# Kernel optimization log

Hardware: AMD Instinct MI355X
Metric: run time of the kernel (lower is better)

Reference implementation:

```python
import jax, jax.numpy as jnp
from jax import lax
import numpy as np

K = 9  # 3x3 kernel taps


def _mdconv(x, w, off_w, off_b):
    # Modulated deformable conv v2, kernel 3x3, stride 1, pad 1, no bias.
    N, C, H, W = x.shape
    # offset/mask predictor: plain 3x3 conv -> 27 channels (18 offsets + 9 mask)
    off = lax.conv_general_dilated(x, off_w, (1, 1), ((1, 1), (1, 1))) + off_b[None, :, None, None]
    o = off[:, :2 * K].reshape(N, K, 2, H, W)  # channel 2k = dy_k, 2k+1 = dx_k
    dy, dx = o[:, :, 0], o[:, :, 1]            # [N,K,H,W]
    m = jax.nn.sigmoid(off[:, 2 * K:])          # modulation mask [N,K,H,W]
    ky = jnp.arange(K) // 3 - 1                 # kernel tap row offsets
    kx = jnp.arange(K) % 3 - 1
    py = dy + ky[None, :, None, None] + jnp.arange(H)[None, None, :, None]
    px = dx + kx[None, :, None, None] + jnp.arange(W)[None, None, None, :]
    y0 = jnp.floor(py)
    x0 = jnp.floor(px)
    ly = py - y0
    lx = px - x0
    y0i = y0.astype(jnp.int32)
    x0i = x0.astype(jnp.int32)
    x_flat = x.reshape(N, C, H * W)

    def corner(yi, xi, wgt):
        valid = (yi >= 0) & (yi < H) & (xi >= 0) & (xi < W)  # zero padding outside
        idx = jnp.clip(yi, 0, H - 1) * W + jnp.clip(xi, 0, W - 1)  # [N,K,H,W]
        g = jax.vmap(lambda xf, ix: xf[:, ix.reshape(-1)])(x_flat, idx)
        g = g.reshape(N, C, K, H, W)
        return g * (wgt * valid)[:, None]

    s = (corner(y0i, x0i, (1 - ly) * (1 - lx))
         + corner(y0i, x0i + 1, (1 - ly) * lx)
         + corner(y0i + 1, x0i, ly * (1 - lx))
         + corner(y0i + 1, x0i + 1, ly * lx))
    s = s * m[:, None]  # modulate sampled values
    return jnp.einsum('nckhw,ock->nohw', s, w.reshape(w.shape[0], C, K))


def _bn_relu(x, g, b, eps=1e-5):
    # training-mode BatchNorm2d (batch statistics over N,H,W) + ReLU
    mu = x.mean((0, 2, 3), keepdims=True)
    var = ((x - mu) ** 2).mean((0, 2, 3), keepdims=True)
    return jax.nn.relu((x - mu) * lax.rsqrt(var + eps) * g[None, :, None, None] + b[None, :, None, None])


def setup_inputs() -> dict:
    key = jax.random.key(0)
    ks = jax.random.split(key, 5)
    N, Cin, Cmid, Cout, H, W = 4, 64, 128, 128, 96, 96
    x = jax.random.normal(ks[0], (N, Cin, H, W), jnp.float32)
    w1 = jax.random.normal(ks[1], (Cmid, Cin, 3, 3), jnp.float32) * 0.06   # ~kaiming scale
    w2 = jax.random.normal(ks[2], (Cout, Cmid, 3, 3), jnp.float32) * 0.04
    off_w1 = jax.random.normal(ks[3], (27, Cin, 3, 3), jnp.float32) * 0.01  # small offsets
    off_w2 = jax.random.normal(ks[4], (27, Cmid, 3, 3), jnp.float32) * 0.01
    return {
        'x': x,
        'w1': w1, 'off_w1': off_w1, 'off_b1': jnp.zeros((27,), jnp.float32),
        'gamma1': jnp.ones((Cmid,), jnp.float32), 'beta1': jnp.zeros((Cmid,), jnp.float32),
        'w2': w2, 'off_w2': off_w2, 'off_b2': jnp.zeros((27,), jnp.float32),
        'gamma2': jnp.ones((Cout,), jnp.float32), 'beta2': jnp.zeros((Cout,), jnp.float32),
    }


def reference(x, w1, off_w1, off_b1, gamma1, beta1, w2, off_w2, off_b2, gamma2, beta2):
    h = _bn_relu(_mdconv(x, w1, off_w1, off_b1), gamma1, beta1)
    return _bn_relu(_mdconv(h, w2, off_w2, off_b2), gamma2, beta2)
```

## Files before the change

kernel.cpp:

```cpp
#include <hip/hip_runtime.h>
#include <math.h>

#define N_  4
#define H_  96
#define W_  96
#define HW  9216
#define NHW 36864
#define O_  128
#define PW  98
#define PHW 9604

typedef unsigned short ushort_t;
typedef __attribute__((ext_vector_type(8))) short bf16x8;
typedef __attribute__((ext_vector_type(4))) float f32x4;
typedef __attribute__((ext_vector_type(8))) unsigned short u16x8;

__device__ __forceinline__ float bf2f(ushort_t u) {
  return __uint_as_float(((unsigned int)u) << 16);
}
__device__ __forceinline__ ushort_t f2bf(float f) {
  unsigned int u = __float_as_uint(f);
  u += 0x7fffu + ((u >> 16) & 1u);
  return (ushort_t)(u >> 16);
}

__global__ __launch_bounds__(256) void to_nhwc_pad_kernel(const float* __restrict__ x,
                                                          ushort_t* __restrict__ xp, int C) {
  __shared__ ushort_t L[32][33];
  int ctiles = C >> 5;
  int b = blockIdx.x;
  int ct = b % ctiles;
  int hwt = (b / ctiles) % (HW / 32);
  int n = b / (ctiles * (HW / 32));
  int tx = threadIdx.x & 31, ty = threadIdx.x >> 5;
#pragma unroll
  for (int i = 0; i < 4; ++i) {
    int cl = ty + i * 8;
    L[cl][tx] = f2bf(x[((size_t)(n * C + ct * 32 + cl)) * HW + hwt * 32 + tx]);
  }
  __syncthreads();
#pragma unroll
  for (int i = 0; i < 4; ++i) {
    int hl = ty + i * 8;
    int hw = hwt * 32 + hl;
    int y = hw / W_, xx = hw % W_;
    xp[((size_t)n * PHW + (y + 1) * PW + (xx + 1)) * C + ct * 32 + tx] = L[tx][hl];
  }
}

__global__ void transpose_w_kernel(const float* __restrict__ w,
                                   ushort_t* __restrict__ wB, int C) {
  int K = C * 9;
  int i = blockIdx.x * 256 + threadIdx.x;
  if (i >= 128 * K) return;
  int o = i / K, r = i % K;
  int kk = r / C, c = r % C;
  wB[i] = f2bf(w[(o * C + c) * 9 + kk]);
}

__global__ void transpose_wo_kernel(const float* __restrict__ ow,
                                    ushort_t* __restrict__ wOB, int C) {
  int K = C * 9;
  int i = blockIdx.x * 256 + threadIdx.x;
  if (i >= 32 * K) return;
  int o = i / K, r = i % K;
  int kk = r / C, c = r % C;
  wOB[i] = (o < 27) ? f2bf(ow[(o * C + c) * 9 + kk]) : (ushort_t)0;
}

__device__ __forceinline__ void gll16(const ushort_t* g, ushort_t* l) {
  __builtin_amdgcn_global_load_lds((const __attribute__((address_space(1))) void*)g,
                                   (__attribute__((address_space(3))) void*)l, 16, 0, 0);
}
__device__ __forceinline__ int swz(int row) {
  return (row & 3) ^ ((row >> 2) & 3);
}

template <int C>
__global__ __launch_bounds__(256) void gemm_off_kernel(
    const ushort_t* __restrict__ xp, const ushort_t* __restrict__ B,
    const float* __restrict__ ob, float* __restrict__ offt, int n0) {
  constexpr int K = C * 9;
  __shared__ __align__(16) ushort_t As[64 * 32];
  __shared__ __align__(16) ushort_t Bs[32 * 32];
  int tid = threadIdx.x;
  int m0 = blockIdx.x * 64;
  int lane = tid & 63, wid = tid >> 6;
  f32x4 acc[2];
  acc[0] = (f32x4){0.f, 0.f, 0.f, 0.f};
  acc[1] = (f32x4){0.f, 0.f, 0.f, 0.f};
  int srow = tid >> 2, chl = tid & 3, q = lane >> 4;
  int mg = m0 + srow;
  int nl = mg / HW, hw = mg % HW;
  int y = hw / W_, x = hw % W_;
  const ushort_t* xn = xp + (size_t)(n0 + nl) * PHW * C;
  int pbase = ((y + 1) * PW + (x + 1)) * C;
  int chg = chl ^ swz(srow);
  for (int kt = 0; kt < K; kt += 32) {
    int kk = kt / C, c0 = kt % C;
    int shift = ((kk / 3 - 1) * PW + (kk % 3 - 1)) * C;
    gll16(xn + pbase + shift + c0 + chg * 8, As + tid * 8);
    if (tid < 128) {
      int row = tid >> 2;
      gll16(B + (size_t)row * K + kt + ((tid & 3) ^ swz(row)) * 8, Bs + tid * 8);
    }
    __syncthreads();
    int r = wid * 16 + (lane & 15);
    bf16x8 af = *reinterpret_cast<const bf16x8*>(&As[r * 32 + ((q ^ swz(r)) << 3)]);
#pragma unroll
    for (int oi = 0; oi < 2; ++oi) {
      int rb = oi * 16 + (lane & 15);
      bf16x8 bfr = *reinterpret_cast<const bf16x8*>(&Bs[rb * 32 + ((q ^ swz(rb)) << 3)]);
      acc[oi] = __builtin_amdgcn_mfma_f32_16x16x32_bf16(af, bfr, acc[oi], 0, 0, 0);
    }
    __syncthreads();
  }
#pragma unroll
  for (int oi = 0; oi < 2; ++oi) {
    int o = oi * 16 + (lane & 15);
    if (o < 27) {
      float b = ob[o];
      int mb = n0 * HW + m0 + wid * 16 + ((lane >> 4) << 2);
#pragma unroll
      for (int j = 0; j < 4; ++j)
        offt[(size_t)(mb + j) * 28 + o] = acc[oi][j] + b;
    }
  }
}

template <int C>
__global__ __launch_bounds__(256) void sample_nhwc_kernel(
    const ushort_t* __restrict__ xp, const float* __restrict__ offt,
    ushort_t* __restrict__ s, int n0) {
  constexpr int CH = C / 8;
  int g = blockIdx.x * 256 + threadIdx.x;
  int cc = g % CH;
  int t = g / CH;
  int kk = t % 9;
  int ml = t / 9;
  int nl = ml / HW, hw = ml % HW;
  int h = hw / W_, w = hw % W_;
  const float* op = offt + ((size_t)n0 * HW + ml) * 28;
  float dy = op[2 * kk];
  float dx = op[2 * kk + 1];
  float mo = op[18 + kk];
  float mm = 1.f / (1.f + __expf(-mo));
  float py = dy + (float)(kk / 3 - 1 + h);
  float px = dx + (float)(kk % 3 - 1 + w);
  float fy = floorf(py), fx = floorf(px);
  int y0 = (int)fy, x0 = (int)fx;
  float ly = py - fy, lx = px - fx;
  int y1 = y0 + 1, x1 = x0 + 1;
  bool vy0 = (y0 >= 0) & (y0 < H_), vy1 = (y1 >= 0) & (y1 < H_);
  bool vx0 = (x0 >= 0) & (x0 < W_), vx1 = (x1 >= 0) & (x1 < W_);
  int y0c = min(max(y0, 0), H_ - 1), y1c = min(max(y1, 0), H_ - 1);
  int x0c = min(max(x0, 0), W_ - 1), x1c = min(max(x1, 0), W_ - 1);
  float w00 = (vy0 & vx0) ? (1.f - ly) * (1.f - lx) * mm : 0.f;
  float w01 = (vy0 & vx1) ? (1.f - ly) * lx * mm : 0.f;
  float w10 = (vy1 & vx0) ? ly * (1.f - lx) * mm : 0.f;
  float w11 = (vy1 & vx1) ? ly * lx * mm : 0.f;
  const ushort_t* xb = xp + (size_t)(n0 + nl) * PHW * C + cc * 8;
  const ushort_t* p00 = xb + (size_t)((y0c + 1) * PW + x0c + 1) * C;
  const ushort_t* p01 = xb + (size_t)((y0c + 1) * PW + x1c + 1) * C;
  const ushort_t* p10 = xb + (size_t)((y1c + 1) * PW + x0c + 1) * C;
  const ushort_t* p11 = xb + (size_t)((y1c + 1) * PW + x1c + 1) * C;
  u16x8 a = *reinterpret_cast<const u16x8*>(p00);
  u16x8 b = *reinterpret_cast<const u16x8*>(p01);
  u16x8 c2 = *reinterpret_cast<const u16x8*>(p10);
  u16x8 d = *reinterpret_cast<const u16x8*>(p11);
  u16x8 r;
#pragma unroll
  for (int e = 0; e < 8; ++e) {
    float v = w00 * bf2f(a[e]) + w01 * bf2f(b[e])
            + w10 * bf2f(c2[e]) + w11 * bf2f(d[e]);
    r[e] = f2bf(v);
  }
  *reinterpret_cast<u16x8*>(s + ((size_t)ml * 9 + kk) * C + cc * 8) = r;
}

template <int K>
__global__ __launch_bounds__(256) void gemm_kernel(
    const ushort_t* __restrict__ A, const ushort_t* __restrict__ B,
    float* __restrict__ Y, int mbase) {
  __shared__ __align__(16) ushort_t As[64 * 32];
  __shared__ __align__(16) ushort_t Bs[128 * 32];
  int tid = threadIdx.x;
  int m0 = blockIdx.x * 64;
  int lane = tid & 63, wid = tid >> 6;
  int wr = wid >> 1, wc = wid & 1;
  f32x4 acc[2][4];
#pragma unroll
  for (int mi = 0; mi < 2; ++mi)
#pragma unroll
    for (int oi = 0; oi < 4; ++oi) acc[mi][oi] = (f32x4){0.f, 0.f, 0.f, 0.f};
  int srow = tid >> 2, chl = tid & 3, q = lane >> 4;
  for (int kt = 0; kt < K; kt += 32) {
    gll16(A + (size_t)(m0 + srow) * K + kt + (chl ^ swz(srow)) * 8, As + tid * 8);
#pragma unroll
    for (int rr = 0; rr < 2; ++rr) {
      int row = srow + 64 * rr;
      gll16(B + (size_t)row * K + kt + (chl ^ swz(row)) * 8, Bs + rr * 2048 + tid * 8);
    }
    __syncthreads();
    bf16x8 af[2], bfr[4];
#pragma unroll
    for (int mi = 0; mi < 2; ++mi) {
      int r = wr * 32 + mi * 16 + (lane & 15);
      af[mi] = *reinterpret_cast<const bf16x8*>(&As[r * 32 + ((q ^ swz(r)) << 3)]);
    }
#pragma unroll
    for (int oi = 0; oi < 4; ++oi) {
      int r = wc * 64 + oi * 16 + (lane & 15);
      bfr[oi] = *reinterpret_cast<const bf16x8*>(&Bs[r * 32 + ((q ^ swz(r)) << 3)]);
    }
#pragma unroll
    for (int mi = 0; mi < 2; ++mi)
#pragma unroll
      for (int oi = 0; oi < 4; ++oi)
        acc[mi][oi] = __builtin_amdgcn_mfma_f32_16x16x32_bf16(af[mi], bfr[oi], acc[mi][oi], 0, 0, 0);
    __syncthreads();
  }
#pragma unroll
  for (int mi = 0; mi < 2; ++mi)
#pragma unroll
    for (int oi = 0; oi < 4; ++oi) {
      int o = wc * 64 + oi * 16 + (lane & 15);
      int mb = m0 + wr * 32 + mi * 16 + ((lane >> 4) << 2);
#pragma unroll
      for (int j = 0; j < 4; ++j)
        Y[(size_t)(mbase + mb + j) * O_ + o] = acc[mi][oi][j];
    }
}

__global__ __launch_bounds__(256) void bn_stats_kernel(const float* __restrict__ Y,
                                                       float* __restrict__ stats) {
  int o = threadIdx.x & 127;
  int seg = blockIdx.x * 2 + (threadIdx.x >> 7);
  const float* p = Y + (size_t)seg * 72 * O_ + o;
  float s = 0.f, s2 = 0.f;
#pragma unroll 4
  for (int mm = 0; mm < 72; ++mm) {
    float v = p[(size_t)mm * O_];
    s += v; s2 += v * v;
  }
  atomicAdd(&stats[o], s);
  atomicAdd(&stats[128 + o], s2);
}

__global__ __launch_bounds__(256) void bn_apply_pad_kernel(
    const float* __restrict__ Y, const float* __restrict__ stats,
    const float* __restrict__ gamma, const float* __restrict__ beta,
    ushort_t* __restrict__ hp) {
  int g = blockIdx.x * 256 + threadIdx.x;
  int m = g >> 4;
  int o0 = (g & 15) * 8;
  int n = m / HW, hw = m % HW;
  int y = hw / W_, x = hw % W_;
  const float4* yp = reinterpret_cast<const float4*>(Y) + (size_t)g * 2;
  float4 a = yp[0], b = yp[1];
  float va[8] = {a.x, a.y, a.z, a.w, b.x, b.y, b.z, b.w};
  u16x8 r;
#pragma unroll
  for (int e = 0; e < 8; ++e) {
    int o = o0 + e;
    float mu = stats[o] * (1.f / (float)NHW);
    float var = stats[128 + o] * (1.f / (float)NHW) - mu * mu;
    float sc = rsqrtf(var + 1e-5f) * gamma[o];
    float sh = beta[o] - mu * sc;
    r[e] = f2bf(fmaxf(fmaf(va[e], sc, sh), 0.f));
  }
  size_t pp = ((size_t)n * PHW + (y + 1) * PW + (x + 1)) * 128;
  *reinterpret_cast<u16x8*>(hp + pp + o0) = r;
}

__global__ __launch_bounds__(256) void bn_apply_t_kernel(
    const float* __restrict__ Y, const float* __restrict__ stats,
    const float* __restrict__ gamma, const float* __restrict__ beta,
    float* __restrict__ outf) {
  __shared__ float L[64][129];
  __shared__ float Lsc[128], Lsh[128];
  int tid = threadIdx.x;
  int m0 = blockIdx.x * 64;
  if (tid < 128) {
    float mu = stats[tid] * (1.f / (float)NHW);
    float var = stats[128 + tid] * (1.f / (float)NHW) - mu * mu;
    float sc = rsqrtf(var + 1e-5f) * gamma[tid];
    Lsc[tid] = sc;
    Lsh[tid] = beta[tid] - mu * sc;
  }
#pragma unroll
  for (int it = 0; it < 8; ++it) {
    int idx = it * 256 + tid;
    int ml = idx >> 5, oq = idx & 31;
    float4 v = *reinterpret_cast<const float4*>(&Y[(size_t)(m0 + ml) * O_ + oq * 4]);
    L[ml][oq * 4 + 0] = v.x; L[ml][oq * 4 + 1] = v.y;
    L[ml][oq * 4 + 2] = v.z; L[ml][oq * 4 + 3] = v.w;
  }
  __syncthreads();
  int n = m0 / HW, hw0 = m0 % HW;
#pragma unroll
  for (int it = 0; it < 32; ++it) {
    int idx = it * 256 + tid;
    int ol = idx >> 6, ml = idx & 63;
    float r = fmaxf(fmaf(L[ml][ol], Lsc[ol], Lsh[ol]), 0.f);
    outf[((size_t)n * O_ + ol) * HW + hw0 + ml] = r;
  }
}

extern "C" void kernel_launch(void* const* d_in, const int* in_sizes, int n_in,
                              void* d_out, int out_size, void* d_ws, size_t ws_size,
                              hipStream_t stream) {
  const float* x      = (const float*)d_in[0];
  const float* w1     = (const float*)d_in[1];
  const float* off_w1 = (const float*)d_in[2];
  const float* off_b1 = (const float*)d_in[3];
  const float* gamma1 = (const float*)d_in[4];
  const float* beta1  = (const float*)d_in[5];
  const float* w2     = (const float*)d_in[6];
  const float* off_w2 = (const float*)d_in[7];
  const float* off_b2 = (const float*)d_in[8];
  const float* gamma2 = (const float*)d_in[9];
  const float* beta2  = (const float*)d_in[10];
  float* out = (float*)d_out;

  char* p = (char*)d_ws;
  auto alloc = [&](size_t bytes) -> void* {
    void* r = (void*)p;
    p += (bytes + 255) & ~(size_t)255;
    return r;
  };
  float*    offt  = (float*)alloc((size_t)NHW * 28 * 4);
  float*    Y     = (float*)alloc((size_t)NHW * O_ * 4);
  float*    stats = (float*)alloc(512 * 4);
  ushort_t* wB1   = (ushort_t*)alloc(73728 * 2);
  ushort_t* wB2   = (ushort_t*)alloc(147456 * 2);
  ushort_t* wOB1  = (ushort_t*)alloc(32 * 576 * 2);
  ushort_t* wOB2  = (ushort_t*)alloc(32 * 1152 * 2);
  ushort_t* xp    = (ushort_t*)alloc((size_t)N_ * PHW * 64 * 2);
  ushort_t* hp    = (ushort_t*)alloc((size_t)N_ * PHW * 128 * 2);
  size_t used = (size_t)(p - (char*)d_ws);
  size_t s_full = (size_t)NHW * 1152 * 2;
  int nspan = (ws_size >= used + s_full) ? 4 : 1;
  ushort_t* sbuf = (ushort_t*)p;

  hipMemsetAsync(xp, 0, (size_t)N_ * PHW * 64 * 2, stream);
  hipMemsetAsync(hp, 0, (size_t)N_ * PHW * 128 * 2, stream);
  hipMemsetAsync(stats, 0, 512 * 4, stream);
  to_nhwc_pad_kernel<<<2304, 256, 0, stream>>>(x, xp, 64);
  transpose_w_kernel<<<288, 256, 0, stream>>>(w1, wB1, 64);
  transpose_w_kernel<<<576, 256, 0, stream>>>(w2, wB2, 128);
  transpose_wo_kernel<<<72, 256, 0, stream>>>(off_w1, wOB1, 64);
  transpose_wo_kernel<<<144, 256, 0, stream>>>(off_w2, wOB2, 128);

  for (int n0 = 0; n0 < 4; n0 += nspan) {
    gemm_off_kernel<64><<<nspan * 144, 256, 0, stream>>>(xp, wOB1, off_b1, offt, n0);
    sample_nhwc_kernel<64><<<nspan * 2592, 256, 0, stream>>>(xp, offt, sbuf, n0);
    gemm_kernel<576><<<nspan * 144, 256, 0, stream>>>(sbuf, wB1, Y, n0 * HW);
  }
  bn_stats_kernel<<<256, 256, 0, stream>>>(Y, stats);
  bn_apply_pad_kernel<<<2304, 256, 0, stream>>>(Y, stats, gamma1, beta1, hp);

  for (int n0 = 0; n0 < 4; n0 += nspan) {
    gemm_off_kernel<128><<<nspan * 144, 256, 0, stream>>>(hp, wOB2, off_b2, offt, n0);
    sample_nhwc_kernel<128><<<nspan * 5184, 256, 0, stream>>>(hp, offt, sbuf, n0);
    gemm_kernel<1152><<<nspan * 144, 256, 0, stream>>>(sbuf, wB2, Y, n0 * HW);
  }
  bn_stats_kernel<<<256, 256, 0, stream>>>(Y, stats + 256);
  bn_apply_t_kernel<<<576, 256, 0, stream>>>(Y, stats + 256, gamma2, beta2, out);
}
```

Measured before the change: 263.6 us.

## Fuse BN statistics into GEMM epilogue and double GEMM K-tile to 64

```diff
diff --git a/kernel.cpp b/kernel.cpp
--- a/kernel.cpp
+++ b/kernel.cpp
@@ -181,9 +181,9 @@
 template <int K>
 __global__ __launch_bounds__(256) void gemm_kernel(
     const ushort_t* __restrict__ A, const ushort_t* __restrict__ B,
-    float* __restrict__ Y, int mbase) {
-  __shared__ __align__(16) ushort_t As[64 * 32];
-  __shared__ __align__(16) ushort_t Bs[128 * 32];
+    float* __restrict__ Y, int mbase, float* __restrict__ stats) {
+  __shared__ __align__(16) ushort_t As[64 * 64];
+  __shared__ __align__(16) ushort_t Bs[128 * 64];
   int tid = threadIdx.x;
   int m0 = blockIdx.x * 64;
   int lane = tid & 63, wid = tid >> 6;
@@ -193,31 +193,48 @@
   for (int mi = 0; mi < 2; ++mi)
 #pragma unroll
     for (int oi = 0; oi < 4; ++oi) acc[mi][oi] = (f32x4){0.f, 0.f, 0.f, 0.f};
-  int srow = tid >> 2, chl = tid & 3, q = lane >> 4;
-  for (int kt = 0; kt < K; kt += 32) {
-    gll16(A + (size_t)(m0 + srow) * K + kt + (chl ^ swz(srow)) * 8, As + tid * 8);
+  int srow8 = tid >> 3;
+  int slot = tid & 7;
+  int q = lane >> 4;
+  for (int kt = 0; kt < K; kt += 64) {
 #pragma unroll
     for (int rr = 0; rr < 2; ++rr) {
-      int row = srow + 64 * rr;
-      gll16(B + (size_t)row * K + kt + (chl ^ swz(row)) * 8, Bs + rr * 2048 + tid * 8);
+      int row = rr * 32 + srow8;
+      gll16(A + (size_t)(m0 + row) * K + kt + ((slot ^ (row & 7)) << 3),
+            As + (rr * 256 + tid) * 8);
+    }
+#pragma unroll
+    for (int rr = 0; rr < 4; ++rr) {
+      int row = rr * 32 + srow8;
+      gll16(B + (size_t)row * K + kt + ((slot ^ (row & 7)) << 3),
+            Bs + (rr * 256 + tid) * 8);
     }
     __syncthreads();
-    bf16x8 af[2], bfr[4];
+    bf16x8 af[2][2], bfr[4][2];
 #pragma unroll
     for (int mi = 0; mi < 2; ++mi) {
       int r = wr * 32 + mi * 16 + (lane & 15);
-      af[mi] = *reinterpret_cast<const bf16x8*>(&As[r * 32 + ((q ^ swz(r)) << 3)]);
+#pragma unroll
+      for (int ks = 0; ks < 2; ++ks)
+        af[mi][ks] = *reinterpret_cast<const bf16x8*>(
+            &As[r * 64 + (((ks * 4 + q) ^ (r & 7)) << 3)]);
     }
 #pragma unroll
     for (int oi = 0; oi < 4; ++oi) {
       int r = wc * 64 + oi * 16 + (lane & 15);
-      bfr[oi] = *reinterpret_cast<const bf16x8*>(&Bs[r * 32 + ((q ^ swz(r)) << 3)]);
-    }
-#pragma unroll
-    for (int mi = 0; mi < 2; ++mi)
-#pragma unroll
-      for (int oi = 0; oi < 4; ++oi)
-        acc[mi][oi] = __builtin_amdgcn_mfma_f32_16x16x32_bf16(af[mi], bfr[oi], acc[mi][oi], 0, 0, 0);
+#pragma unroll
+      for (int ks = 0; ks < 2; ++ks)
+        bfr[oi][ks] = *reinterpret_cast<const bf16x8*>(
+            &Bs[r * 64 + (((ks * 4 + q) ^ (r & 7)) << 3)]);
+    }
+#pragma unroll
+    for (int ks = 0; ks < 2; ++ks)
+#pragma unroll
+      for (int mi = 0; mi < 2; ++mi)
+#pragma unroll
+        for (int oi = 0; oi < 4; ++oi)
+          acc[mi][oi] = __builtin_amdgcn_mfma_f32_16x16x32_bf16(
+              af[mi][ks], bfr[oi][ks], acc[mi][oi], 0, 0, 0);
     __syncthreads();
   }
 #pragma unroll
@@ -230,21 +247,24 @@
       for (int j = 0; j < 4; ++j)
         Y[(size_t)(mbase + mb + j) * O_ + o] = acc[mi][oi][j];
     }
-}
-
-__global__ __launch_bounds__(256) void bn_stats_kernel(const float* __restrict__ Y,
-                                                       float* __restrict__ stats) {
-  int o = threadIdx.x & 127;
-  int seg = blockIdx.x * 2 + (threadIdx.x >> 7);
-  const float* p = Y + (size_t)seg * 72 * O_ + o;
-  float s = 0.f, s2 = 0.f;
-#pragma unroll 4
-  for (int mm = 0; mm < 72; ++mm) {
-    float v = p[(size_t)mm * O_];
-    s += v; s2 += v * v;
-  }
-  atomicAdd(&stats[o], s);
-  atomicAdd(&stats[128 + o], s2);
+#pragma unroll
+  for (int oi = 0; oi < 4; ++oi) {
+    float s = 0.f, s2 = 0.f;
+#pragma unroll
+    for (int mi = 0; mi < 2; ++mi)
+#pragma unroll
+      for (int j = 0; j < 4; ++j) {
+        float v = acc[mi][oi][j];
+        s += v; s2 += v * v;
+      }
+    s  += __shfl_xor(s, 16);  s  += __shfl_xor(s, 32);
+    s2 += __shfl_xor(s2, 16); s2 += __shfl_xor(s2, 32);
+    if ((lane >> 4) == 0) {
+      int o = wc * 64 + oi * 16 + (lane & 15);
+      atomicAdd(&stats[o], s);
+      atomicAdd(&stats[128 + o], s2);
+    }
+  }
 }
 
 __global__ __launch_bounds__(256) void bn_apply_pad_kernel(
@@ -343,8 +363,7 @@
   int nspan = (ws_size >= used + s_full) ? 4 : 1;
   ushort_t* sbuf = (ushort_t*)p;
 
-  hipMemsetAsync(xp, 0, (size_t)N_ * PHW * 64 * 2, stream);
-  hipMemsetAsync(hp, 0, (size_t)N_ * PHW * 128 * 2, stream);
+  hipMemsetAsync(xp, 0, (size_t)N_ * PHW * (64 + 128) * 2, stream);
   hipMemsetAsync(stats, 0, 512 * 4, stream);
   to_nhwc_pad_kernel<<<2304, 256, 0, stream>>>(x, xp, 64);
   transpose_w_kernel<<<288, 256, 0, stream>>>(w1, wB1, 64);
@@ -355,16 +374,14 @@
   for (int n0 = 0; n0 < 4; n0 += nspan) {
     gemm_off_kernel<64><<<nspan * 144, 256, 0, stream>>>(xp, wOB1, off_b1, offt, n0);
     sample_nhwc_kernel<64><<<nspan * 2592, 256, 0, stream>>>(xp, offt, sbuf, n0);
-    gemm_kernel<576><<<nspan * 144, 256, 0, stream>>>(sbuf, wB1, Y, n0 * HW);
-  }
-  bn_stats_kernel<<<256, 256, 0, stream>>>(Y, stats);
+    gemm_kernel<576><<<nspan * 144, 256, 0, stream>>>(sbuf, wB1, Y, n0 * HW, stats);
+  }
   bn_apply_pad_kernel<<<2304, 256, 0, stream>>>(Y, stats, gamma1, beta1, hp);
 
   for (int n0 = 0; n0 < 4; n0 += nspan) {
     gemm_off_kernel<128><<<nspan * 144, 256, 0, stream>>>(hp, wOB2, off_b2, offt, n0);
     sample_nhwc_kernel<128><<<nspan * 5184, 256, 0, stream>>>(hp, offt, sbuf, n0);
-    gemm_kernel<1152><<<nspan * 144, 256, 0, stream>>>(sbuf, wB2, Y, n0 * HW);
-  }
-  bn_stats_kernel<<<256, 256, 0, stream>>>(Y, stats + 256);
+    gemm_kernel<1152><<<nspan * 144, 256, 0, stream>>>(sbuf, wB2, Y, n0 * HW, stats + 256);
+  }
   bn_apply_t_kernel<<<576, 256, 0, stream>>>(Y, stats + 256, gamma2, beta2, out);
 }
```

Result: slower. 270.3 us (+2.5%).

## Fuse bilinear sampling into GEMM A-tile load and BN stats into epilogue

Applied to the files above, without the earlier changes.

```diff
diff --git a/kernel.cpp b/kernel.cpp
--- a/kernel.cpp
+++ b/kernel.cpp
@@ -79,7 +79,7 @@
 template <int C>
 __global__ __launch_bounds__(256) void gemm_off_kernel(
     const ushort_t* __restrict__ xp, const ushort_t* __restrict__ B,
-    const float* __restrict__ ob, float* __restrict__ offt, int n0) {
+    const float* __restrict__ ob, float* __restrict__ offt) {
   constexpr int K = C * 9;
   __shared__ __align__(16) ushort_t As[64 * 32];
   __shared__ __align__(16) ushort_t Bs[32 * 32];
@@ -93,7 +93,7 @@
   int mg = m0 + srow;
   int nl = mg / HW, hw = mg % HW;
   int y = hw / W_, x = hw % W_;
-  const ushort_t* xn = xp + (size_t)(n0 + nl) * PHW * C;
+  const ushort_t* xn = xp + (size_t)nl * PHW * C;
   int pbase = ((y + 1) * PW + (x + 1)) * C;
   int chg = chl ^ swz(srow);
   for (int kt = 0; kt < K; kt += 32) {
@@ -120,7 +120,7 @@
     int o = oi * 16 + (lane & 15);
     if (o < 27) {
       float b = ob[o];
-      int mb = n0 * HW + m0 + wid * 16 + ((lane >> 4) << 2);
+      int mb = m0 + wid * 16 + ((lane >> 4) << 2);
 #pragma unroll
       for (int j = 0; j < 4; ++j)
         offt[(size_t)(mb + j) * 28 + o] = acc[oi][j] + b;
@@ -129,59 +129,11 @@
 }
 
 template <int C>
-__global__ __launch_bounds__(256) void sample_nhwc_kernel(
+__global__ __launch_bounds__(256) void gemm_fused_kernel(
     const ushort_t* __restrict__ xp, const float* __restrict__ offt,
-    ushort_t* __restrict__ s, int n0) {
-  constexpr int CH = C / 8;
-  int g = blockIdx.x * 256 + threadIdx.x;
-  int cc = g % CH;
-  int t = g / CH;
-  int kk = t % 9;
-  int ml = t / 9;
-  int nl = ml / HW, hw = ml % HW;
-  int h = hw / W_, w = hw % W_;
-  const float* op = offt + ((size_t)n0 * HW + ml) * 28;
-  float dy = op[2 * kk];
-  float dx = op[2 * kk + 1];
-  float mo = op[18 + kk];
-  float mm = 1.f / (1.f + __expf(-mo));
-  float py = dy + (float)(kk / 3 - 1 + h);
-  float px = dx + (float)(kk % 3 - 1 + w);
-  float fy = floorf(py), fx = floorf(px);
-  int y0 = (int)fy, x0 = (int)fx;
-  float ly = py - fy, lx = px - fx;
-  int y1 = y0 + 1, x1 = x0 + 1;
-  bool vy0 = (y0 >= 0) & (y0 < H_), vy1 = (y1 >= 0) & (y1 < H_);
-  bool vx0 = (x0 >= 0) & (x0 < W_), vx1 = (x1 >= 0) & (x1 < W_);
-  int y0c = min(max(y0, 0), H_ - 1), y1c = min(max(y1, 0), H_ - 1);
-  int x0c = min(max(x0, 0), W_ - 1), x1c = min(max(x1, 0), W_ - 1);
-  float w00 = (vy0 & vx0) ? (1.f - ly) * (1.f - lx) * mm : 0.f;
-  float w01 = (vy0 & vx1) ? (1.f - ly) * lx * mm : 0.f;
-  float w10 = (vy1 & vx0) ? ly * (1.f - lx) * mm : 0.f;
-  float w11 = (vy1 & vx1) ? ly * lx * mm : 0.f;
-  const ushort_t* xb = xp + (size_t)(n0 + nl) * PHW * C + cc * 8;
-  const ushort_t* p00 = xb + (size_t)((y0c + 1) * PW + x0c + 1) * C;
-  const ushort_t* p01 = xb + (size_t)((y0c + 1) * PW + x1c + 1) * C;
-  const ushort_t* p10 = xb + (size_t)((y1c + 1) * PW + x0c + 1) * C;
-  const ushort_t* p11 = xb + (size_t)((y1c + 1) * PW + x1c + 1) * C;
-  u16x8 a = *reinterpret_cast<const u16x8*>(p00);
-  u16x8 b = *reinterpret_cast<const u16x8*>(p01);
-  u16x8 c2 = *reinterpret_cast<const u16x8*>(p10);
-  u16x8 d = *reinterpret_cast<const u16x8*>(p11);
-  u16x8 r;
-#pragma unroll
-  for (int e = 0; e < 8; ++e) {
-    float v = w00 * bf2f(a[e]) + w01 * bf2f(b[e])
-            + w10 * bf2f(c2[e]) + w11 * bf2f(d[e]);
-    r[e] = f2bf(v);
-  }
-  *reinterpret_cast<u16x8*>(s + ((size_t)ml * 9 + kk) * C + cc * 8) = r;
-}
-
-template <int K>
-__global__ __launch_bounds__(256) void gemm_kernel(
-    const ushort_t* __restrict__ A, const ushort_t* __restrict__ B,
-    float* __restrict__ Y, int mbase) {
+    const ushort_t* __restrict__ B, float* __restrict__ Y,
+    float* __restrict__ stats) {
+  constexpr int K = C * 9;
   __shared__ __align__(16) ushort_t As[64 * 32];
   __shared__ __align__(16) ushort_t Bs[128 * 32];
   int tid = threadIdx.x;
@@ -194,24 +146,68 @@
 #pragma unroll
     for (int oi = 0; oi < 4; ++oi) acc[mi][oi] = (f32x4){0.f, 0.f, 0.f, 0.f};
   int srow = tid >> 2, chl = tid & 3, q = lane >> 4;
+  int mg = m0 + srow;
+  int n = mg / HW, hw = mg % HW;
+  int h = hw / W_, w = hw % W_;
+  const float* op = offt + (size_t)mg * 28;
+  const ushort_t* xb = xp + (size_t)n * PHW * C;
+  const ushort_t *p00 = xb, *p01 = xb, *p10 = xb, *p11 = xb;
+  float w00 = 0.f, w01 = 0.f, w10 = 0.f, w11 = 0.f;
+  int wslot = (chl ^ swz(srow)) << 3;
+
   for (int kt = 0; kt < K; kt += 32) {
-    gll16(A + (size_t)(m0 + srow) * K + kt + (chl ^ swz(srow)) * 8, As + tid * 8);
+    int kk = kt / C, c0 = kt % C;
+    if (c0 == 0) {
+      float dy = op[2 * kk], dx = op[2 * kk + 1], mo = op[18 + kk];
+      float mm = 1.f / (1.f + __expf(-mo));
+      float py = dy + (float)(kk / 3 - 1 + h);
+      float px = dx + (float)(kk % 3 - 1 + w);
+      float fy = floorf(py), fx = floorf(px);
+      int y0 = (int)fy, x0 = (int)fx;
+      float ly = py - fy, lx = px - fx;
+      int y1 = y0 + 1, x1 = x0 + 1;
+      bool vy0 = (y0 >= 0) & (y0 < H_), vy1 = (y1 >= 0) & (y1 < H_);
+      bool vx0 = (x0 >= 0) & (x0 < W_), vx1 = (x1 >= 0) & (x1 < W_);
+      int y0c = min(max(y0, 0), H_ - 1), y1c = min(max(y1, 0), H_ - 1);
+      int x0c = min(max(x0, 0), W_ - 1), x1c = min(max(x1, 0), W_ - 1);
+      w00 = (vy0 & vx0) ? (1.f - ly) * (1.f - lx) * mm : 0.f;
+      w01 = (vy0 & vx1) ? (1.f - ly) * lx * mm : 0.f;
+      w10 = (vy1 & vx0) ? ly * (1.f - lx) * mm : 0.f;
+      w11 = (vy1 & vx1) ? ly * lx * mm : 0.f;
+      p00 = xb + (size_t)((y0c + 1) * PW + x0c + 1) * C;
+      p01 = xb + (size_t)((y0c + 1) * PW + x1c + 1) * C;
+      p10 = xb + (size_t)((y1c + 1) * PW + x0c + 1) * C;
+      p11 = xb + (size_t)((y1c + 1) * PW + x1c + 1) * C;
+    }
 #pragma unroll
     for (int rr = 0; rr < 2; ++rr) {
       int row = srow + 64 * rr;
-      gll16(B + (size_t)row * K + kt + (chl ^ swz(row)) * 8, Bs + rr * 2048 + tid * 8);
-    }
+      gll16(B + (size_t)row * K + kt + ((chl ^ swz(row)) << 3), Bs + rr * 2048 + tid * 8);
+    }
+    int c = c0 + chl * 8;
+    u16x8 va = *reinterpret_cast<const u16x8*>(p00 + c);
+    u16x8 vb = *reinterpret_cast<const u16x8*>(p01 + c);
+    u16x8 vc = *reinterpret_cast<const u16x8*>(p10 + c);
+    u16x8 vd = *reinterpret_cast<const u16x8*>(p11 + c);
+    u16x8 r;
+#pragma unroll
+    for (int e = 0; e < 8; ++e) {
+      float v = w00 * bf2f(va[e]) + w01 * bf2f(vb[e])
+              + w10 * bf2f(vc[e]) + w11 * bf2f(vd[e]);
+      r[e] = f2bf(v);
+    }
+    *reinterpret_cast<u16x8*>(&As[srow * 32 + wslot]) = r;
     __syncthreads();
     bf16x8 af[2], bfr[4];
 #pragma unroll
     for (int mi = 0; mi < 2; ++mi) {
-      int r = wr * 32 + mi * 16 + (lane & 15);
-      af[mi] = *reinterpret_cast<const bf16x8*>(&As[r * 32 + ((q ^ swz(r)) << 3)]);
+      int rr2 = wr * 32 + mi * 16 + (lane & 15);
+      af[mi] = *reinterpret_cast<const bf16x8*>(&As[rr2 * 32 + ((q ^ swz(rr2)) << 3)]);
     }
 #pragma unroll
     for (int oi = 0; oi < 4; ++oi) {
-      int r = wc * 64 + oi * 16 + (lane & 15);
-      bfr[oi] = *reinterpret_cast<const bf16x8*>(&Bs[r * 32 + ((q ^ swz(r)) << 3)]);
+      int rr2 = wc * 64 + oi * 16 + (lane & 15);
+      bfr[oi] = *reinterpret_cast<const bf16x8*>(&Bs[rr2 * 32 + ((q ^ swz(rr2)) << 3)]);
     }
 #pragma unroll
     for (int mi = 0; mi < 2; ++mi)
@@ -228,23 +224,26 @@
       int mb = m0 + wr * 32 + mi * 16 + ((lane >> 4) << 2);
 #pragma unroll
       for (int j = 0; j < 4; ++j)
-        Y[(size_t)(mbase + mb + j) * O_ + o] = acc[mi][oi][j];
-    }
-}
-
-__global__ __launch_bounds__(256) void bn_stats_kernel(const float* __restrict__ Y,
-                                                       float* __restrict__ stats) {
-  int o = threadIdx.x & 127;
-  int seg = blockIdx.x * 2 + (threadIdx.x >> 7);
-  const float* p = Y + (size_t)seg * 72 * O_ + o;
-  float s = 0.f, s2 = 0.f;
-#pragma unroll 4
-  for (int mm = 0; mm < 72; ++mm) {
-    float v = p[(size_t)mm * O_];
-    s += v; s2 += v * v;
-  }
-  atomicAdd(&stats[o], s);
-  atomicAdd(&stats[128 + o], s2);
+        Y[(size_t)(mb + j) * O_ + o] = acc[mi][oi][j];
+    }
+#pragma unroll
+  for (int oi = 0; oi < 4; ++oi) {
+    float s = 0.f, s2 = 0.f;
+#pragma unroll
+    for (int mi = 0; mi < 2; ++mi)
+#pragma unroll
+      for (int j = 0; j < 4; ++j) {
+        float v = acc[mi][oi][j];
+        s += v; s2 += v * v;
+      }
+    s  += __shfl_xor(s, 16);  s  += __shfl_xor(s, 32);
+    s2 += __shfl_xor(s2, 16); s2 += __shfl_xor(s2, 32);
+    if ((lane >> 4) == 0) {
+      int o = wc * 64 + oi * 16 + (lane & 15);
+      atomicAdd(&stats[o], s);
+      atomicAdd(&stats[128 + o], s2);
+    }
+  }
 }
 
 __global__ __launch_bounds__(256) void bn_apply_pad_kernel(
@@ -338,13 +337,8 @@
   ushort_t* wOB2  = (ushort_t*)alloc(32 * 1152 * 2);
   ushort_t* xp    = (ushort_t*)alloc((size_t)N_ * PHW * 64 * 2);
   ushort_t* hp    = (ushort_t*)alloc((size_t)N_ * PHW * 128 * 2);
-  size_t used = (size_t)(p - (char*)d_ws);
-  size_t s_full = (size_t)NHW * 1152 * 2;
-  int nspan = (ws_size >= used + s_full) ? 4 : 1;
-  ushort_t* sbuf = (ushort_t*)p;
-
-  hipMemsetAsync(xp, 0, (size_t)N_ * PHW * 64 * 2, stream);
-  hipMemsetAsync(hp, 0, (size_t)N_ * PHW * 128 * 2, stream);
+
+  hipMemsetAsync(xp, 0, (size_t)N_ * PHW * (64 + 128) * 2, stream);
   hipMemsetAsync(stats, 0, 512 * 4, stream);
   to_nhwc_pad_kernel<<<2304, 256, 0, stream>>>(x, xp, 64);
   transpose_w_kernel<<<288, 256, 0, stream>>>(w1, wB1, 64);
@@ -352,19 +346,11 @@
   transpose_wo_kernel<<<72, 256, 0, stream>>>(off_w1, wOB1, 64);
   transpose_wo_kernel<<<144, 256, 0, stream>>>(off_w2, wOB2, 128);
 
-  for (int n0 = 0; n0 < 4; n0 += nspan) {
-    gemm_off_kernel<64><<<nspan * 144, 256, 0, stream>>>(xp, wOB1, off_b1, offt, n0);
-    sample_nhwc_kernel<64><<<nspan * 2592, 256, 0, stream>>>(xp, offt, sbuf, n0);
-    gemm_kernel<576><<<nspan * 144, 256, 0, stream>>>(sbuf, wB1, Y, n0 * HW);
-  }
-  bn_stats_kernel<<<256, 256, 0, stream>>>(Y, stats);
+  gemm_off_kernel<64><<<576, 256, 0, stream>>>(xp, wOB1, off_b1, offt);
+  gemm_fused_kernel<64><<<576, 256, 0, stream>>>(xp, offt, wB1, Y, stats);
   bn_apply_pad_kernel<<<2304, 256, 0, stream>>>(Y, stats, gamma1, beta1, hp);
 
-  for (int n0 = 0; n0 < 4; n0 += nspan) {
-    gemm_off_kernel<128><<<nspan * 144, 256, 0, stream>>>(hp, wOB2, off_b2, offt, n0);
-    sample_nhwc_kernel<128><<<nspan * 5184, 256, 0, stream>>>(hp, offt, sbuf, n0);
-    gemm_kernel<1152><<<nspan * 144, 256, 0, stream>>>(sbuf, wB2, Y, n0 * HW);
-  }
-  bn_stats_kernel<<<256, 256, 0, stream>>>(Y, stats + 256);
+  gemm_off_kernel<128><<<576, 256, 0, stream>>>(hp, wOB2, off_b2, offt);
+  gemm_fused_kernel<128><<<576, 256, 0, stream>>>(hp, offt, wB2, Y, stats + 256);
   bn_apply_t_kernel<<<576, 256, 0, stream>>>(Y, stats + 256, gamma2, beta2, out);
 }
```

After: 258.4 us. 1.02x faster.
